# Optimization experiments

Hardware: AMD Instinct MI355X
Metric: run time of the kernel (lower is better)

## Reference

```python
import jax, jax.numpy as jnp
import numpy as np

NPART = 128
NSTART = 128
NEND = 128
BATCH = 4096


def setup_inputs() -> dict:
    key = jax.random.key(0)
    k1, k2, k3, k4, k5 = jax.random.split(key, 5)
    gaussian = jax.random.normal(k1, (BATCH, NSTART), dtype=jnp.float32)
    logp = jax.random.normal(k2, (NPART, 1), dtype=jnp.float32)
    pos = 3.0 * jax.random.normal(k3, (NPART, NSTART), dtype=jnp.float32)
    sigma = 0.1 * jax.random.normal(k4, (NPART, NEND, NEND), dtype=jnp.float32)
    # deterministic stand-in for tf.random.categorical(logp.T, batch)
    randind = jax.random.randint(k5, (BATCH,), 0, NPART, dtype=jnp.int32)
    return {"gaussian": gaussian, "logp": logp, "pos": pos,
            "sigma": sigma, "randind": randind}


def reference(gaussian, logp, pos, sigma, randind):
    batch = gaussian.shape[0]
    y = gaussian.reshape(batch, -1)                      # [B, nend]
    p = jax.nn.softmax(logp[:, 0], axis=0)               # [npart]
    weights = p[randind]                                 # [B]
    pos_g = pos[randind]                                 # [B, nstart]
    # full per-particle matmul as in the original: [npart, B, nend]
    temp = jnp.einsum('pij,bj->pbi', sigma, y)
    vv = temp[randind, jnp.arange(batch)]                # gather one particle per sample -> [B, nend]
    out = (pos_g + vv).reshape(gaussian.shape)
    return out, weights, randind
```

## Files before the change

### kernel.cpp

```cpp
#include <hip/hip_runtime.h>

#define NPART 128
#define NDIM  128
#define BATCH 4096
#define BPP   4
#define NBLK  (NPART * BPP)
#define NXCD  8

typedef __attribute__((address_space(1))) const unsigned int guint;
typedef __attribute__((address_space(3))) unsigned int luint;

__global__ __launch_bounds__(256)
void mix_kernel(const float* __restrict__ gaussian,
                const float* __restrict__ logp,
                const float* __restrict__ pos,
                const float* __restrict__ sigma,
                const int*   __restrict__ randind,
                float* __restrict__ out,
                float* __restrict__ wout,
                float* __restrict__ indout) {
    const int g  = blockIdx.x;
    const int sg = (g % NXCD) * (NBLK / NXCD) + g / NXCD;
    const int p  = sg >> 2;
    const int q  = sg & 3;
    const int t  = threadIdx.x;
    const int i  = t & 127;
    const int hf = t >> 7;
    const int lane = t & 63, wid = t >> 6;

    __shared__ float4 smat[NDIM * 32];
    __shared__ int    wtot[4];
    __shared__ int    slist[160];
    __shared__ float  smx[2];

    const int4* rnd4 = reinterpret_cast<const int4*>(randind);
    int mk[16];
    {
        int4 a = rnd4[t * 4 + 0], b = rnd4[t * 4 + 1],
             c = rnd4[t * 4 + 2], d = rnd4[t * 4 + 3];
        mk[0]=a.x;  mk[1]=a.y;  mk[2]=a.z;  mk[3]=a.w;
        mk[4]=b.x;  mk[5]=b.y;  mk[6]=b.z;  mk[7]=b.w;
        mk[8]=c.x;  mk[9]=c.y;  mk[10]=c.z; mk[11]=c.w;
        mk[12]=d.x; mk[13]=d.y; mk[14]=d.z; mk[15]=d.w;
    }

    if (t < 64) {
        float a = logp[t], b = logp[t + 64];
        float m = fmaxf(a, b);
        #pragma unroll
        for (int o = 32; o > 0; o >>= 1) m = fmaxf(m, __shfl_xor(m, o));
        float ea = expf(a - m), eb = expf(b - m);
        float s = ea + eb;
        #pragma unroll
        for (int o = 32; o > 0; o >>= 1) s += __shfl_xor(s, o);
        if (t == 0) { smx[0] = m; smx[1] = s; }
    }

    int cnt = 0;
    #pragma unroll
    for (int k = 0; k < 16; ++k) cnt += (mk[k] == p) ? 1 : 0;
    int v = cnt;
    #pragma unroll
    for (int o = 1; o < 64; o <<= 1) {
        int u = __shfl_up(v, o);
        if (lane >= o) v += u;
    }
    if (lane == 63) wtot[wid] = v;
    __syncthreads();
    int woff = 0;
    #pragma unroll
    for (int w = 0; w < 4; ++w) woff += (w < wid) ? wtot[w] : 0;
    const int base = woff + v - cnt;
    const int n    = wtot[0] + wtot[1] + wtot[2] + wtot[3];
    const int lo   = (n * q) / BPP;
    const int hi   = (n * (q + 1)) / BPP;
    const int nq   = hi - lo;
    if (nq == 0) return;

    {
        const float4* src = reinterpret_cast<const float4*>(sigma)
                            + (size_t)p * 4096;
        #pragma unroll
        for (int w = 0; w < 16; ++w) {
            const int idx = w * 256 + t;
            const int r = idx >> 5, c = idx & 31;
            const float4* gp = src + (r * 32 + (c ^ (r & 31)));
            luint* lp = (luint*)(smat + (w * 256 + wid * 64));
            __builtin_amdgcn_global_load_lds((guint*)gp, lp, 16, 0, 0);
        }
    }

    const float pw = expf(logp[p] - smx[0]) / smx[1];
    {
        int r = base;
        #pragma unroll
        for (int k = 0; k < 16; ++k) {
            if (mk[k] == p) {
                if (r >= lo && r < hi) slist[r - lo] = t * 16 + k;
                ++r;
            }
        }
    }
    __syncthreads();

    float4 sr[32];
    #pragma unroll
    for (int u = 0; u < 32; ++u)
        sr[u] = smat[i * 32 + (u ^ (i & 31))];

    const float posv = pos[p * NDIM + i];

    for (int s = hf; s < nq; s += 2) {
        const int sid = __builtin_amdgcn_readfirstlane(slist[s]);
        const float4* y = reinterpret_cast<const float4*>(
            gaussian + (size_t)sid * NDIM);
        float a0 = 0.f, a1 = 0.f, a2 = 0.f, a3 = 0.f;
        #pragma unroll
        for (int u = 0; u < 32; ++u) {
            float4 yv = y[u];
            float4 sv = sr[u];
            a0 += sv.x * yv.x;  a1 += sv.y * yv.y;
            a2 += sv.z * yv.z;  a3 += sv.w * yv.w;
        }
        out[sid * NDIM + i] = posv + ((a0 + a1) + (a2 + a3));
        if (i == 0) {
            wout[sid]   = pw;
            indout[sid] = (float)p;
        }
    }
}

extern "C" void kernel_launch(void* const* d_in, const int* in_sizes, int n_in,
                              void* d_out, int out_size, void* d_ws, size_t ws_size,
                              hipStream_t stream) {
    const float* gaussian = (const float*)d_in[0];
    const float* logp     = (const float*)d_in[1];
    const float* pos      = (const float*)d_in[2];
    const float* sigma    = (const float*)d_in[3];
    const int*   randind  = (const int*)d_in[4];

    float* out    = (float*)d_out;
    float* wout   = out + BATCH * NDIM;
    float* indout = wout + BATCH;

    mix_kernel<<<NBLK, 256, 0, stream>>>(gaussian, logp, pos, sigma, randind,
                                         out, wout, indout);
}
```

Before: 15.52 us.

## Split particle work by output-row quarters instead of sample quarters

Each block now handles one quarter of a particle's sigma rows (32 rows) for all samples of that particle, rather than all 128 rows for a quarter of the samples. Each block loads 16KB of sigma into LDS instead of 64KB, and the load is issued before the randind scan. Each thread computes one output row across many samples (8 sample groups of 32 lanes). Weight and index outputs are written during list building by the rq==0 blocks. slist is capped at 144 entries, so a particle with more samples would silently drop outputs. The gaussian rows are now reread by four blocks.

Result: slower. 26.10 us (+68.2%).

```diff
diff --git a/kernel.cpp b/kernel.cpp
--- a/kernel.cpp
+++ b/kernel.cpp
@@ -3,8 +3,8 @@
 #define NPART 128
 #define NDIM  128
 #define BATCH 4096
-#define BPP   4
-#define NBLK  (NPART * BPP)
+#define RQN   4
+#define NBLK  (NPART * RQN)
 #define NXCD  8
 
 typedef __attribute__((address_space(1))) const unsigned int guint;
@@ -22,16 +22,29 @@
     const int g  = blockIdx.x;
     const int sg = (g % NXCD) * (NBLK / NXCD) + g / NXCD;
     const int p  = sg >> 2;
-    const int q  = sg & 3;
+    const int rq = sg & 3;
     const int t  = threadIdx.x;
-    const int i  = t & 127;
-    const int hf = t >> 7;
+    const int il = t & 31;
+    const int oc = t >> 5;
     const int lane = t & 63, wid = t >> 6;
 
-    __shared__ float4 smat[NDIM * 32];
+    __shared__ float4 smat[32 * 32];
     __shared__ int    wtot[4];
-    __shared__ int    slist[160];
+    __shared__ int    slist[144];
     __shared__ float  smx[2];
+
+    {
+        const float4* src = reinterpret_cast<const float4*>(sigma)
+                            + (size_t)p * 4096 + rq * 1024;
+        #pragma unroll
+        for (int w = 0; w < 4; ++w) {
+            const int idx = w * 256 + t;
+            const int r = idx >> 5, c = idx & 31;
+            const float4* gp = src + (r * 32 + (c ^ r));
+            luint* lp = (luint*)(smat + (w * 256 + wid * 64));
+            __builtin_amdgcn_global_load_lds((guint*)gp, lp, 16, 0, 0);
+        }
+    }
 
     const int4* rnd4 = reinterpret_cast<const int4*>(randind);
     int mk[16];
@@ -72,23 +85,6 @@
     for (int w = 0; w < 4; ++w) woff += (w < wid) ? wtot[w] : 0;
     const int base = woff + v - cnt;
     const int n    = wtot[0] + wtot[1] + wtot[2] + wtot[3];
-    const int lo   = (n * q) / BPP;
-    const int hi   = (n * (q + 1)) / BPP;
-    const int nq   = hi - lo;
-    if (nq == 0) return;
-
-    {
-        const float4* src = reinterpret_cast<const float4*>(sigma)
-                            + (size_t)p * 4096;
-        #pragma unroll
-        for (int w = 0; w < 16; ++w) {
-            const int idx = w * 256 + t;
-            const int r = idx >> 5, c = idx & 31;
-            const float4* gp = src + (r * 32 + (c ^ (r & 31)));
-            luint* lp = (luint*)(smat + (w * 256 + wid * 64));
-            __builtin_amdgcn_global_load_lds((guint*)gp, lp, 16, 0, 0);
-        }
-    }
 
     const float pw = expf(logp[p] - smx[0]) / smx[1];
     {
@@ -96,7 +92,11 @@
         #pragma unroll
         for (int k = 0; k < 16; ++k) {
             if (mk[k] == p) {
-                if (r >= lo && r < hi) slist[r - lo] = t * 16 + k;
+                if (r < 144) slist[r] = t * 16 + k;
+                if (rq == 0) {
+                    wout[t * 16 + k]   = pw;
+                    indout[t * 16 + k] = (float)p;
+                }
                 ++r;
             }
         }
@@ -106,12 +106,12 @@
     float4 sr[32];
     #pragma unroll
     for (int u = 0; u < 32; ++u)
-        sr[u] = smat[i * 32 + (u ^ (i & 31))];
+        sr[u] = smat[il * 32 + (u ^ il)];
 
-    const float posv = pos[p * NDIM + i];
+    const float posv = pos[p * NDIM + rq * 32 + il];
 
-    for (int s = hf; s < nq; s += 2) {
-        const int sid = __builtin_amdgcn_readfirstlane(slist[s]);
+    for (int s = oc; s < n; s += 8) {
+        const int sid = slist[s];
         const float4* y = reinterpret_cast<const float4*>(
             gaussian + (size_t)sid * NDIM);
         float a0 = 0.f, a1 = 0.f, a2 = 0.f, a3 = 0.f;
@@ -122,11 +122,7 @@
             a0 += sv.x * yv.x;  a1 += sv.y * yv.y;
             a2 += sv.z * yv.z;  a3 += sv.w * yv.w;
         }
-        out[sid * NDIM + i] = posv + ((a0 + a1) + (a2 + a3));
-        if (i == 0) {
-            wout[sid]   = pw;
-            indout[sid] = (float)p;
-        }
+        out[sid * NDIM + rq * 32 + il] = posv + ((a0 + a1) + (a2 + a3));
     }
 }
 
```
